# Kernel tuning notes

Measured on AMD Instinct MI355X. Metric: run time of the kernel, lower is better.

## Reference

```python
import jax, jax.numpy as jnp
import numpy as np
from jax import lax

K = 16  # knn_k


def _mlp(x, W1, b1, W2, b2):
    h = jax.nn.gelu(x @ W1 + b1, approximate=False)  # torch nn.GELU default = exact
    return h @ W2 + b2


def setup_inputs() -> dict:
    key = jax.random.key(0)
    ks = jax.random.split(key, 10)
    B, N, F, H = 8, 4096, 64, 128

    def xav(k, shape):
        fan_in = shape[0]
        return (jax.random.normal(k, shape, jnp.float32) / np.sqrt(fan_in)).astype(jnp.float32)

    return {
        "coords": jax.random.normal(ks[0], (B, N, 3), jnp.float32),
        "features": jax.random.normal(ks[1], (B, N, F), jnp.float32),
        "inv_W1": xav(ks[2], (6, H)), "inv_b1": jnp.zeros((H,), jnp.float32),
        "inv_W2": xav(ks[3], (H, H)), "inv_b2": jnp.zeros((H,), jnp.float32),
        "feat_W1": xav(ks[4], (F, H)), "feat_b1": jnp.zeros((H,), jnp.float32),
        "feat_W2": xav(ks[5], (H, H)), "feat_b2": jnp.zeros((H,), jnp.float32),
        "sh_W1": xav(ks[6], (2 * H, H)), "sh_b1": jnp.zeros((H,), jnp.float32),
        "sh_W2": xav(ks[7], (H, H)), "sh_b2": jnp.zeros((H,), jnp.float32),
        "g0_W": xav(ks[8], (H, 1)), "g0_b": jnp.zeros((1,), jnp.float32),
    }


def _local_geometry(coords):
    # coords: [B,N,3]
    B, N, _ = coords.shape
    k = min(K, N - 1)
    # squared pairwise distances (monotone in euclidean dist -> same kNN indices)
    sq = jnp.sum(coords * coords, axis=-1)                    # [B,N]
    dist2 = sq[:, :, None] + sq[:, None, :] - 2.0 * jnp.einsum("bnd,bmd->bnm", coords, coords)
    dist2 = lax.stop_gradient(dist2)
    eye = jnp.eye(N, dtype=bool)
    dist2 = jnp.where(eye[None], jnp.inf, dist2)
    _, idx = lax.top_k(-dist2, k)                             # smallest-k -> [B,N,k]
    neighbors = jax.vmap(lambda c, i: c[i])(coords, idx)      # [B,N,k,3]
    relative = neighbors - coords[:, :, None, :]              # [B,N,k,3]
    cov = jnp.einsum("bnki,bnkj->bnij", relative, relative) / float(k)  # [B,N,3,3]
    evals, evecs = jnp.linalg.eigh(cov)                       # ascending
    normals = evecs[..., 0]                                   # smallest-eigval eigenvector, [B,N,3]
    center = coords.mean(axis=1, keepdims=True)
    outward = coords - center
    orient = jnp.sign(jnp.sum(normals * outward, axis=-1, keepdims=True))
    orient = jnp.where(orient == 0, 1.0, orient)
    normals = normals * orient
    normals = normals / jnp.maximum(jnp.linalg.norm(normals, axis=-1, keepdims=True), 1e-6)
    radius = jnp.linalg.norm(relative, axis=-1).mean(axis=-1, keepdims=True)   # [B,N,1]
    centered_radius = jnp.linalg.norm(outward, axis=-1, keepdims=True)
    eig_sum = jnp.maximum(evals.sum(axis=-1, keepdims=True), 1e-6)
    dominance = evals[..., 2:3] / eig_sum
    invariants = jnp.concatenate([evals, radius, centered_radius, dominance], axis=-1)  # [B,N,6]
    return normals, invariants


def reference(coords, features, inv_W1, inv_b1, inv_W2, inv_b2,
              feat_W1, feat_b1, feat_W2, feat_b2,
              sh_W1, sh_b1, sh_W2, sh_b2, g0_W, g0_b):
    normals, invariants = _local_geometry(coords)
    inv_h = _mlp(invariants, inv_W1, inv_b1, inv_W2, inv_b2)
    feat_h = _mlp(features, feat_W1, feat_b1, feat_W2, feat_b2)
    hidden = _mlp(jnp.concatenate([inv_h, feat_h], axis=-1), sh_W1, sh_b1, sh_W2, sh_b2)
    scalar = hidden @ g0_W + g0_b                                   # grade 0, [B,N,1]
    plane = jnp.stack([normals[..., 0], normals[..., 1], -normals[..., 2],
                       -jnp.sum(coords * normals, axis=-1)], axis=-1)  # grade 1, [B,N,4]
    biv = jnp.concatenate([normals, jnp.zeros_like(normals)], axis=-1)  # grade 2, [B,N,6]
    point = jnp.concatenate([coords, jnp.ones(coords.shape[:-1] + (1,), coords.dtype)], axis=-1)  # grade 3 OPNS point
    zero4 = jnp.zeros(coords.shape[:-1] + (1,), coords.dtype)            # grade 4
    return jnp.concatenate([scalar, plane, biv, point, zero4], axis=-1)  # [B,N,16]
```

## Files before the change

kernel.cpp:

```cpp
#include <hip/hip_runtime.h>
#include <hip/hip_bf16.h>

#define BB 8
#define NN 4096
#define FF 64
#define HH 128
#define KNN 16

typedef __attribute__((ext_vector_type(8))) short bf16x8;
typedef __attribute__((ext_vector_type(4))) float f32x4;

#define OFF_iW2 0
#define OFF_fW1 16384
#define OFF_fW2 24576
#define OFF_sW1 40960
#define OFF_sW2 73728
#define HI_SZ   90112

__device__ __forceinline__ float sq3(float x, float y, float z) {
    return fmaf(z, z, fmaf(y, y, __fmul_rn(x, x)));
}
__device__ __forceinline__ float dist2f(float px, float py, float pz, float psq, float4 cc) {
    float t = fmaf(pz, cc.z, fmaf(py, cc.y, __fmul_rn(px, cc.x)));
    return __fsub_rn(__fadd_rn(psq, cc.w), __fmul_rn(2.0f, t));
}

__device__ __forceinline__ short f2bf(float x) {
    unsigned u = __float_as_uint(x);
    u += 0x7fffu + ((u >> 16) & 1u);
    return (short)(u >> 16);
}
__device__ __forceinline__ float bf2f(short s) {
    return __uint_as_float(((unsigned)(unsigned short)s) << 16);
}

extern "C" __global__ __launch_bounds__(256)
void k_prep(const float* __restrict__ coords, float4* __restrict__ coords4, float* __restrict__ center) {
    const int b = blockIdx.x, tid = threadIdx.x;
    __shared__ float rx[256], ry[256], rz[256];
    float sx = 0.f, sy = 0.f, sz = 0.f;
    for (int n = tid; n < NN; n += 256) {
        const float* c = coords + (size_t)(b * NN + n) * 3;
        float x = c[0], y = c[1], z = c[2];
        coords4[b * NN + n] = make_float4(x, y, z, sq3(x, y, z));
        sx += x; sy += y; sz += z;
    }
    rx[tid] = sx; ry[tid] = sy; rz[tid] = sz;
    __syncthreads();
    for (int s = 128; s > 0; s >>= 1) {
        if (tid < s) { rx[tid] += rx[tid + s]; ry[tid] += ry[tid + s]; rz[tid] += rz[tid + s]; }
        __syncthreads();
    }
    if (tid == 0) {
        center[b * 4 + 0] = rx[0] * (1.0f / NN);
        center[b * 4 + 1] = ry[0] * (1.0f / NN);
        center[b * 4 + 2] = rz[0] * (1.0f / NN);
    }
}

extern "C" __global__ __launch_bounds__(256)
void k_wprep(const float* __restrict__ iW2, const float* __restrict__ fW1,
             const float* __restrict__ fW2, const float* __restrict__ sW1,
             const float* __restrict__ sW2, short* __restrict__ wbf) {
    const int w = blockIdx.y;
    const float* W; int K; int off;
    if (w == 0)      { W = iW2; K = 128; off = OFF_iW2; }
    else if (w == 1) { W = fW1; K = 64;  off = OFF_fW1; }
    else if (w == 2) { W = fW2; K = 128; off = OFF_fW2; }
    else if (w == 3) { W = sW1; K = 256; off = OFF_sW1; }
    else             { W = sW2; K = 128; off = OFF_sW2; }
    short* hi = wbf + off;
    short* lo = wbf + HI_SZ + off;
    const int total = K * 128;
    for (int e = blockIdx.x * 256 + threadIdx.x; e < total; e += gridDim.x * 256) {
        int j = e & 7, lane = (e >> 3) & 63, ct = (e >> 9) & 7, kb = e >> 12;
        int k = kb * 32 + (lane >> 4) * 8 + j;
        int n = ct * 16 + (lane & 15);
        float v = W[k * 128 + n];
        short h = f2bf(v);
        float r = v - bf2f(h);
        hi[e] = h; lo[e] = f2bf(r);
    }
}

#define JROT(app, aqq, apq, arp, arq, vp0, vp1, vp2, vq0, vq1, vq2) { \
    float tau_ = (aqq - app) / (2.0f * apq); \
    float tt_ = copysignf(1.0f, tau_) / (fabsf(tau_) + sqrtf(1.0f + tau_ * tau_)); \
    if (apq == 0.0f) tt_ = 0.0f; \
    float cc_ = 1.0f / sqrtf(1.0f + tt_ * tt_); \
    float ss_ = tt_ * cc_; \
    float app_n = cc_*cc_*app - 2.0f*cc_*ss_*apq + ss_*ss_*aqq; \
    float aqq_n = ss_*ss_*app + 2.0f*cc_*ss_*apq + cc_*cc_*aqq; \
    float apq_n = cc_*ss_*(app - aqq) + (cc_*cc_ - ss_*ss_)*apq; \
    float arp_n = cc_*arp - ss_*arq; \
    float arq_n = ss_*arp + cc_*arq; \
    app = app_n; aqq = aqq_n; apq = apq_n; arp = arp_n; arq = arq_n; \
    float t0_ = cc_*vp0 - ss_*vq0, t1_ = cc_*vp1 - ss_*vq1, t2_ = cc_*vp2 - ss_*vq2; \
    vq0 = ss_*vp0 + cc_*vq0; vq1 = ss_*vp1 + cc_*vq1; vq2 = ss_*vp2 + cc_*vq2; \
    vp0 = t0_; vp1 = t1_; vp2 = t2_; }

#define SWAPF(a, b) { float sw_ = a; a = b; b = sw_; }

__device__ __forceinline__ void sort16(float (&d)[16]) {
#pragma unroll
    for (int k = 2; k <= 16; k <<= 1) {
#pragma unroll
        for (int j = k >> 1; j > 0; j >>= 1) {
#pragma unroll
            for (int i = 0; i < 16; i++) {
                int l = i ^ j;
                if (l > i) {
                    if ((i & k) == 0) {
                        float mn = fminf(d[i], d[l]);
                        d[l] = fmaxf(d[i], d[l]);
                        d[i] = mn;
                    } else {
                        float mx = fmaxf(d[i], d[l]);
                        d[l] = fminf(d[i], d[l]);
                        d[i] = mx;
                    }
                }
            }
        }
    }
}

__device__ __forceinline__ void merge16(float (&dk)[16], const float (&d)[16]) {
    float t[16];
#pragma unroll
    for (int i = 0; i < 16; i++) t[i] = fminf(dk[i], d[15 - i]);
#pragma unroll
    for (int j = 8; j > 0; j >>= 1) {
#pragma unroll
        for (int i = 0; i < 16; i++) {
            int l = i ^ j;
            if (l > i) {
                float mn = fminf(t[i], t[l]);
                t[l] = fmaxf(t[i], t[l]);
                t[i] = mn;
            }
        }
    }
#pragma unroll
    for (int i = 0; i < 16; i++) dk[i] = t[i];
}

__device__ __forceinline__ float gelu_exact(float x) {
    return 0.5f * x * (1.0f + erff(x * 0.70710678118654752440f));
}

template <int KDIM, int LDA>
__device__ __forceinline__ void gemm_small(const float* A, const float* __restrict__ W,
                                           const float* __restrict__ bias, int p0, int c0, float acc[4][4]) {
    float4 bb = *(const float4*)(bias + c0);
#pragma unroll
    for (int i = 0; i < 4; i++) { acc[i][0] = bb.x; acc[i][1] = bb.y; acc[i][2] = bb.z; acc[i][3] = bb.w; }
#pragma unroll
    for (int k = 0; k < KDIM; k++) {
        float4 w = *(const float4*)(W + k * HH + c0);
#pragma unroll
        for (int i = 0; i < 4; i++) {
            float a = A[(p0 + i) * LDA + k];
            acc[i][0] = fmaf(a, w.x, acc[i][0]);
            acc[i][1] = fmaf(a, w.y, acc[i][1]);
            acc[i][2] = fmaf(a, w.z, acc[i][2]);
            acc[i][3] = fmaf(a, w.w, acc[i][3]);
        }
    }
}

template <int KB, bool INIT>
__device__ __forceinline__ void gemm_mfma(const short* Ab, const short* __restrict__ whi,
                                          const short* __restrict__ wlo,
                                          const float* __restrict__ bias,
                                          int wid, int lane, f32x4 acc[2][2]) {
    const int m16 = lane & 15, quad = lane >> 4;
    if (INIT) {
        float b0 = bias[(wid * 2 + 0) * 16 + m16];
        float b1 = bias[(wid * 2 + 1) * 16 + m16];
        acc[0][0] = (f32x4){b0, b0, b0, b0}; acc[1][0] = acc[0][0];
        acc[0][1] = (f32x4){b1, b1, b1, b1}; acc[1][1] = acc[0][1];
    }
#pragma unroll 1
    for (int kb = 0; kb < KB; kb++) {
        bf16x8 a0 = *(const bf16x8*)(Ab + m16 * 136 + kb * 32 + quad * 8);
        bf16x8 a1 = *(const bf16x8*)(Ab + (m16 + 16) * 136 + kb * 32 + quad * 8);
#pragma unroll
        for (int c = 0; c < 2; c++) {
            const int off = ((kb * 8 + wid * 2 + c) * 64 + lane) * 8;
            bf16x8 bh = *(const bf16x8*)(whi + off);
            bf16x8 bl = *(const bf16x8*)(wlo + off);
            acc[0][c] = __builtin_amdgcn_mfma_f32_16x16x32_bf16(a0, bh, acc[0][c], 0, 0, 0);
            acc[0][c] = __builtin_amdgcn_mfma_f32_16x16x32_bf16(a0, bl, acc[0][c], 0, 0, 0);
            acc[1][c] = __builtin_amdgcn_mfma_f32_16x16x32_bf16(a1, bh, acc[1][c], 0, 0, 0);
            acc[1][c] = __builtin_amdgcn_mfma_f32_16x16x32_bf16(a1, bl, acc[1][c], 0, 0, 0);
        }
    }
}

__device__ __forceinline__ void acc_to_bf(short* dst, f32x4 acc[2][2], int wid, int lane, bool dogelu) {
    const int m16 = lane & 15, quad = lane >> 4;
#pragma unroll
    for (int mt = 0; mt < 2; mt++)
#pragma unroll
        for (int c = 0; c < 2; c++)
#pragma unroll
            for (int i = 0; i < 4; i++) {
                float v = acc[mt][c][i];
                if (dogelu) v = gelu_exact(v);
                dst[(mt * 16 + quad * 4 + i) * 136 + (wid * 2 + c) * 16 + m16] = f2bf(v);
            }
}

extern "C" __global__ __launch_bounds__(256, 7)
void k_fused(const float4* __restrict__ coords4, const float* __restrict__ center,
             const float* __restrict__ features, const short* __restrict__ wbf,
             const float* __restrict__ iW1, const float* __restrict__ ib1,
             const float* __restrict__ ib2,
             const float* __restrict__ fb1, const float* __restrict__ fb2,
             const float* __restrict__ sb1, const float* __restrict__ sb2,
             const float* __restrict__ gW, const float* __restrict__ gb,
             float* __restrict__ out) {
    const int blk = blockIdx.x;
    const int b = blk >> 7;
    const int chunk = blk & 127;
    const int tid = threadIdx.x;
    const int pid = tid & 31;
    const int h = tid >> 5;
    const int n = chunk * 32 + pid;
    const float4* __restrict__ C = coords4 + b * NN;

    __shared__ __align__(16) char smem[22144];
    float4* tile = (float4*)smem;
    short* ilist = (short*)(smem + 8192);
    int* cnts = (int*)(smem + 19968);
    float* inv8 = (float*)(smem + 20992);
    float* sc = (float*)(smem + 22016);
    float* mb = (float*)smem;
    short* Abf = (short*)smem;
    short* FHbf = (short*)(smem + 8704);

    float4 me = C[n];
    const float px = me.x, py = me.y, pz = me.z, psq = me.w;
    const float INF = __builtin_inff();

    float dk[KNN];
#pragma unroll
    for (int i = 0; i < KNN; i++) dk[i] = INF;

    for (int r = 0; r < 8; r++) {
        __syncthreads();
#pragma unroll
        for (int e = tid; e < 512; e += 256) {
            int seg = e >> 6, idx = e & 63;
            tile[e] = C[seg * 512 + r * 64 + idx];
        }
        __syncthreads();
        const float4* T = &tile[h * 64];
        const int selfj = n - (h * 512 + r * 64);
#pragma unroll
        for (int bt = 0; bt < 4; bt++) {
            float d[16];
#pragma unroll
            for (int i = 0; i < 16; i++) {
                float4 cc = T[bt * 16 + i];
                float dd = dist2f(px, py, pz, psq, cc);
                d[i] = (bt * 16 + i) == selfj ? INF : dd;
            }
            sort16(d);
            merge16(dk, d);
        }
    }

    __syncthreads();
#pragma unroll
    for (int i = 0; i < KNN; i++) mb[tid * 17 + i] = dk[i];
    __syncthreads();
#pragma unroll
    for (int p = 1; p < 8; p++) {
        const int partner = (((h + p) & 7) << 5) + pid;
        float o[16];
#pragma unroll
        for (int i = 0; i < KNN; i++) o[i] = mb[partner * 17 + i];
        merge16(dk, o);
    }
    const float d15 = dk[15];

    int cs = 0, ct = 0;
    const int lbase = (pid * 8 + h) * 23;
    for (int r = 0; r < 8; r++) {
        __syncthreads();
#pragma unroll
        for (int e = tid; e < 512; e += 256) {
            int seg = e >> 6, idx = e & 63;
            tile[e] = C[seg * 512 + r * 64 + idx];
        }
        __syncthreads();
        const float4* T = &tile[h * 64];
        const int base = h * 512 + r * 64;
#pragma unroll 4
        for (int j = 0; j < 64; j++) {
            float4 cc = T[j];
            float d = dist2f(px, py, pz, psq, cc);
            int g = base + j;
            if (g != n && d <= d15) {
                if (d < d15) {
                    if (cs < 15) ilist[lbase + cs] = (short)g;
                    cs++;
                } else if (ct < 8) {
                    ilist[lbase + 15 + ct] = (short)g;
                    ct++;
                }
            }
        }
    }
    cnts[pid * 8 + h] = (cs & 0xff) | (ct << 8);
    __syncthreads();

    if (h == 0) {
        int s[8], t8[8], sb[8], tb[8], cum[8], tcum[8];
#pragma unroll
        for (int q = 0; q < 8; q++) {
            int cp = cnts[pid * 8 + q];
            s[q] = cp & 0xff; t8[q] = cp >> 8;
            sb[q] = (pid * 8 + q) * 23; tb[q] = sb[q] + 15;
        }
        cum[0] = s[0]; tcum[0] = t8[0];
#pragma unroll
        for (int q = 1; q < 8; q++) { cum[q] = cum[q - 1] + s[q]; tcum[q] = tcum[q - 1] + t8[q]; }

        float cxx = 0.f, cxy = 0.f, cxz = 0.f, cyy = 0.f, cyz = 0.f, czz = 0.f, radsum = 0.f;
#pragma unroll
        for (int j = 0; j < KNN; j++) {
            int addr = sb[0] + j;
#pragma unroll
            for (int q = 1; q < 8; q++)
                if (j >= cum[q - 1]) addr = sb[q] + (j - cum[q - 1]);
            int jt = j - cum[7];
            if (j >= cum[7]) addr = tb[0] + jt;
#pragma unroll
            for (int q = 1; q < 8; q++)
                if (j >= cum[7] && jt >= tcum[q - 1]) addr = tb[q] + (jt - tcum[q - 1]);
            int id = ilist[addr];
            float4 cc = C[id];
            float rx = __fsub_rn(cc.x, px), ry = __fsub_rn(cc.y, py), rz = __fsub_rn(cc.z, pz);
            cxx = __fadd_rn(cxx, __fmul_rn(rx, rx));
            cxy = __fadd_rn(cxy, __fmul_rn(rx, ry));
            cxz = __fadd_rn(cxz, __fmul_rn(rx, rz));
            cyy = __fadd_rn(cyy, __fmul_rn(ry, ry));
            cyz = __fadd_rn(cyz, __fmul_rn(ry, rz));
            czz = __fadd_rn(czz, __fmul_rn(rz, rz));
            float rr = __fadd_rn(__fadd_rn(__fmul_rn(rx, rx), __fmul_rn(ry, ry)), __fmul_rn(rz, rz));
            radsum = __fadd_rn(radsum, sqrtf(rr));
        }
        const float inv_k = 1.0f / KNN;
        float a00 = cxx * inv_k, a01 = cxy * inv_k, a02 = cxz * inv_k;
        float a11 = cyy * inv_k, a12 = cyz * inv_k, a22 = czz * inv_k;

        float V00 = 1.f, V01 = 0.f, V02 = 0.f;
        float V10 = 0.f, V11 = 1.f, V12 = 0.f;
        float V20 = 0.f, V21 = 0.f, V22 = 1.f;
        for (int sweep = 0; sweep < 6; sweep++) {
            JROT(a00, a11, a01, a02, a12, V00, V10, V20, V01, V11, V21);
            JROT(a00, a22, a02, a01, a12, V00, V10, V20, V02, V12, V22);
            JROT(a11, a22, a12, a01, a02, V01, V11, V21, V02, V12, V22);
        }
        float e0 = a00, e1 = a11, e2 = a22;
        float x0 = V00, y0 = V10, z0 = V20;
        float x1 = V01, y1 = V11, z1 = V21;
        float x2 = V02, y2 = V12, z2 = V22;
        if (e0 > e1) { SWAPF(e0, e1); SWAPF(x0, x1); SWAPF(y0, y1); SWAPF(z0, z1); }
        if (e1 > e2) { SWAPF(e1, e2); SWAPF(x1, x2); SWAPF(y1, y2); SWAPF(z1, z2); }
        if (e0 > e1) { SWAPF(e0, e1); SWAPF(x0, x1); SWAPF(y0, y1); SWAPF(z0, z1); }

        float cx = center[b * 4 + 0], cy = center[b * 4 + 1], cz = center[b * 4 + 2];
        float ox = __fsub_rn(px, cx), oy = __fsub_rn(py, cy), oz = __fsub_rn(pz, cz);
        float dt = __fadd_rn(__fadd_rn(__fmul_rn(x0, ox), __fmul_rn(y0, oy)), __fmul_rn(z0, oz));
        float sgn = (dt >= 0.0f) ? 1.0f : -1.0f;
        x0 *= sgn; y0 *= sgn; z0 *= sgn;
        float nrm = sqrtf(__fadd_rn(__fadd_rn(__fmul_rn(x0, x0), __fmul_rn(y0, y0)), __fmul_rn(z0, z0)));
        float den = fmaxf(nrm, 1e-6f);
        x0 = x0 / den; y0 = y0 / den; z0 = z0 / den;

        float radius = radsum * inv_k;
        float crad = sqrtf(__fadd_rn(__fadd_rn(__fmul_rn(ox, ox), __fmul_rn(oy, oy)), __fmul_rn(oz, oz)));
        float esum = fmaxf(__fadd_rn(__fadd_rn(e0, e1), e2), 1e-6f);
        float dom = e2 / esum;

        float* ip = inv8 + pid * 8;
        ip[0] = e0; ip[1] = e1; ip[2] = e2; ip[3] = radius; ip[4] = crad; ip[5] = dom;
        ip[6] = 0.f; ip[7] = 0.f;

        float pd = __fadd_rn(__fadd_rn(__fmul_rn(px, x0), __fmul_rn(py, y0)), __fmul_rn(pz, z0));
        float4* o = (float4*)(out + (size_t)(b * NN + n) * 16);
        o[0] = make_float4(0.0f, x0, y0, -z0);
        o[1] = make_float4(-pd, x0, y0, z0);
        o[2] = make_float4(0.0f, 0.0f, 0.0f, px);
        o[3] = make_float4(py, pz, 1.0f, 0.0f);
        sc[pid] = gb[0];
    }
    __syncthreads();

    const int wid = tid >> 6, lane = tid & 63;
    const short* w_iW2h = wbf + OFF_iW2; const short* w_iW2l = wbf + HI_SZ + OFF_iW2;
    const short* w_fW1h = wbf + OFF_fW1; const short* w_fW1l = wbf + HI_SZ + OFF_fW1;
    const short* w_fW2h = wbf + OFF_fW2; const short* w_fW2l = wbf + HI_SZ + OFF_fW2;
    const short* w_sW1h = wbf + OFF_sW1; const short* w_sW1l = wbf + HI_SZ + OFF_sW1;
    const short* w_sW2h = wbf + OFF_sW2; const short* w_sW2l = wbf + HI_SZ + OFF_sW2;
    f32x4 acc[2][2];

    {
        int row = tid >> 3, c8 = (tid & 7) * 8;
        const float* s = features + (size_t)(b * NN + chunk * 32 + row) * FF + c8;
        float4 v0 = *(const float4*)s, v1 = *(const float4*)(s + 4);
        bf16x8 pk;
        pk[0] = f2bf(v0.x); pk[1] = f2bf(v0.y); pk[2] = f2bf(v0.z); pk[3] = f2bf(v0.w);
        pk[4] = f2bf(v1.x); pk[5] = f2bf(v1.y); pk[6] = f2bf(v1.z); pk[7] = f2bf(v1.w);
        *(bf16x8*)(Abf + row * 136 + c8) = pk;
    }
    __syncthreads();

    gemm_mfma<2, true>(Abf, w_fW1h, w_fW1l, fb1, wid, lane, acc);
    __syncthreads();
    acc_to_bf(Abf, acc, wid, lane, true);
    __syncthreads();

    gemm_mfma<4, true>(Abf, w_fW2h, w_fW2l, fb2, wid, lane, acc);
    __syncthreads();
    acc_to_bf(FHbf, acc, wid, lane, false);
    __syncthreads();

    {
        const int cg = tid & 31, pg = tid >> 5;
        const int c0 = cg * 4, p0 = pg * 4;
        float a4[4][4];
        gemm_small<6, 8>(inv8, iW1, ib1, p0, c0, a4);
#pragma unroll
        for (int i = 0; i < 4; i++)
#pragma unroll
            for (int j = 0; j < 4; j++)
                Abf[(p0 + i) * 136 + c0 + j] = f2bf(gelu_exact(a4[i][j]));
    }
    __syncthreads();

    gemm_mfma<4, true>(Abf, w_iW2h, w_iW2l, ib2, wid, lane, acc);
    __syncthreads();
    acc_to_bf(Abf, acc, wid, lane, false);
    __syncthreads();

    gemm_mfma<4, true>(Abf, w_sW1h, w_sW1l, sb1, wid, lane, acc);
    gemm_mfma<4, false>(FHbf, w_sW1h + 16384, w_sW1l + 16384, nullptr, wid, lane, acc);
    __syncthreads();
    acc_to_bf(Abf, acc, wid, lane, true);
    __syncthreads();

    gemm_mfma<4, true>(Abf, w_sW2h, w_sW2l, sb2, wid, lane, acc);
    {
        const int m16 = lane & 15, quad = lane >> 4;
#pragma unroll
        for (int mt = 0; mt < 2; mt++)
#pragma unroll
            for (int c = 0; c < 2; c++) {
                float g = gW[(wid * 2 + c) * 16 + m16];
#pragma unroll
                for (int i = 0; i < 4; i++)
                    atomicAdd(&sc[mt * 16 + quad * 4 + i], acc[mt][c][i] * g);
            }
    }
    __syncthreads();
    if (tid < 32) out[(size_t)(b * NN + n) * 16] = sc[tid];
}

extern "C" void kernel_launch(void* const* d_in, const int* in_sizes, int n_in,
                              void* d_out, int out_size, void* d_ws, size_t ws_size,
                              hipStream_t stream) {
    const float* coords   = (const float*)d_in[0];
    const float* features = (const float*)d_in[1];
    const float* iW1 = (const float*)d_in[2],  * ib1 = (const float*)d_in[3];
    const float* iW2 = (const float*)d_in[4],  * ib2 = (const float*)d_in[5];
    const float* fW1 = (const float*)d_in[6],  * fb1 = (const float*)d_in[7];
    const float* fW2 = (const float*)d_in[8],  * fb2 = (const float*)d_in[9];
    const float* sW1 = (const float*)d_in[10], * sb1 = (const float*)d_in[11];
    const float* sW2 = (const float*)d_in[12], * sb2 = (const float*)d_in[13];
    const float* gW  = (const float*)d_in[14], * gb  = (const float*)d_in[15];
    float* out = (float*)d_out;

    float* ws = (float*)d_ws;
    float4* coords4 = (float4*)ws;
    float* center = ws + BB * NN * 4;
    short* wbf = (short*)((char*)d_ws + 524416);

    hipLaunchKernelGGL(k_prep, dim3(BB), dim3(256), 0, stream, coords, coords4, center);
    hipLaunchKernelGGL(k_wprep, dim3(16, 5), dim3(256), 0, stream, iW2, fW1, fW2, sW1, sW2, wbf);
    hipLaunchKernelGGL(k_fused, dim3(1024), dim3(256), 0, stream, coords4, center, features, wbf,
                       iW1, ib1, ib2, fb1, fb2, sb1, sb2, gW, gb, out);
}
```

Before: 290.1 us.

## Halve points per block to 16 and split kNN scan into 16 segments

Each block now handles 16 query points instead of 32, with 16 threads per point scanning 256-candidate segments. The grid doubles to 2048 blocks, and the tile rows are padded to 33 entries. The MLP stage switches to single 16-row MFMA tiles, and the merge and gather steps are widened to 16 partial lists. The aim is more parallelism and better wave occupancy across CUs. In exchange, each block does more merge work (15 partner merges), every block reloads the weights, and half the threads sit idle during the feature load.

```diff
diff --git a/kernel.cpp b/kernel.cpp
--- a/kernel.cpp
+++ b/kernel.cpp
@@ -150,16 +150,16 @@
 }
 
 template <int KDIM, int LDA>
-__device__ __forceinline__ void gemm_small(const float* A, const float* __restrict__ W,
-                                           const float* __restrict__ bias, int p0, int c0, float acc[4][4]) {
+__device__ __forceinline__ void gemm_small2(const float* A, const float* __restrict__ W,
+                                            const float* __restrict__ bias, int p0, int c0, float acc[2][4]) {
     float4 bb = *(const float4*)(bias + c0);
 #pragma unroll
-    for (int i = 0; i < 4; i++) { acc[i][0] = bb.x; acc[i][1] = bb.y; acc[i][2] = bb.z; acc[i][3] = bb.w; }
+    for (int i = 0; i < 2; i++) { acc[i][0] = bb.x; acc[i][1] = bb.y; acc[i][2] = bb.z; acc[i][3] = bb.w; }
 #pragma unroll
     for (int k = 0; k < KDIM; k++) {
         float4 w = *(const float4*)(W + k * HH + c0);
 #pragma unroll
-        for (int i = 0; i < 4; i++) {
+        for (int i = 0; i < 2; i++) {
             float a = A[(p0 + i) * LDA + k];
             acc[i][0] = fmaf(a, w.x, acc[i][0]);
             acc[i][1] = fmaf(a, w.y, acc[i][1]);
@@ -170,46 +170,41 @@
 }
 
 template <int KB, bool INIT>
-__device__ __forceinline__ void gemm_mfma(const short* Ab, const short* __restrict__ whi,
-                                          const short* __restrict__ wlo,
-                                          const float* __restrict__ bias,
-                                          int wid, int lane, f32x4 acc[2][2]) {
+__device__ __forceinline__ void gemm_mfma16(const short* Ab, const short* __restrict__ whi,
+                                            const short* __restrict__ wlo,
+                                            const float* __restrict__ bias,
+                                            int wid, int lane, f32x4 acc[2]) {
     const int m16 = lane & 15, quad = lane >> 4;
     if (INIT) {
         float b0 = bias[(wid * 2 + 0) * 16 + m16];
         float b1 = bias[(wid * 2 + 1) * 16 + m16];
-        acc[0][0] = (f32x4){b0, b0, b0, b0}; acc[1][0] = acc[0][0];
-        acc[0][1] = (f32x4){b1, b1, b1, b1}; acc[1][1] = acc[0][1];
+        acc[0] = (f32x4){b0, b0, b0, b0};
+        acc[1] = (f32x4){b1, b1, b1, b1};
     }
 #pragma unroll 1
     for (int kb = 0; kb < KB; kb++) {
         bf16x8 a0 = *(const bf16x8*)(Ab + m16 * 136 + kb * 32 + quad * 8);
-        bf16x8 a1 = *(const bf16x8*)(Ab + (m16 + 16) * 136 + kb * 32 + quad * 8);
 #pragma unroll
         for (int c = 0; c < 2; c++) {
             const int off = ((kb * 8 + wid * 2 + c) * 64 + lane) * 8;
             bf16x8 bh = *(const bf16x8*)(whi + off);
             bf16x8 bl = *(const bf16x8*)(wlo + off);
-            acc[0][c] = __builtin_amdgcn_mfma_f32_16x16x32_bf16(a0, bh, acc[0][c], 0, 0, 0);
-            acc[0][c] = __builtin_amdgcn_mfma_f32_16x16x32_bf16(a0, bl, acc[0][c], 0, 0, 0);
-            acc[1][c] = __builtin_amdgcn_mfma_f32_16x16x32_bf16(a1, bh, acc[1][c], 0, 0, 0);
-            acc[1][c] = __builtin_amdgcn_mfma_f32_16x16x32_bf16(a1, bl, acc[1][c], 0, 0, 0);
-        }
-    }
-}
-
-__device__ __forceinline__ void acc_to_bf(short* dst, f32x4 acc[2][2], int wid, int lane, bool dogelu) {
+            acc[c] = __builtin_amdgcn_mfma_f32_16x16x32_bf16(a0, bh, acc[c], 0, 0, 0);
+            acc[c] = __builtin_amdgcn_mfma_f32_16x16x32_bf16(a0, bl, acc[c], 0, 0, 0);
+        }
+    }
+}
+
+__device__ __forceinline__ void acc_to_bf(short* dst, f32x4 acc[2], int wid, int lane, bool dogelu) {
     const int m16 = lane & 15, quad = lane >> 4;
 #pragma unroll
-    for (int mt = 0; mt < 2; mt++)
-#pragma unroll
-        for (int c = 0; c < 2; c++)
-#pragma unroll
-            for (int i = 0; i < 4; i++) {
-                float v = acc[mt][c][i];
-                if (dogelu) v = gelu_exact(v);
-                dst[(mt * 16 + quad * 4 + i) * 136 + (wid * 2 + c) * 16 + m16] = f2bf(v);
-            }
+    for (int c = 0; c < 2; c++)
+#pragma unroll
+        for (int i = 0; i < 4; i++) {
+            float v = acc[c][i];
+            if (dogelu) v = gelu_exact(v);
+            dst[(quad * 4 + i) * 136 + (wid * 2 + c) * 16 + m16] = f2bf(v);
+        }
 }
 
 extern "C" __global__ __launch_bounds__(256, 7)
@@ -222,23 +217,23 @@
              const float* __restrict__ gW, const float* __restrict__ gb,
              float* __restrict__ out) {
     const int blk = blockIdx.x;
-    const int b = blk >> 7;
-    const int chunk = blk & 127;
+    const int b = blk >> 8;
+    const int chunk = blk & 255;
     const int tid = threadIdx.x;
-    const int pid = tid & 31;
-    const int h = tid >> 5;
-    const int n = chunk * 32 + pid;
+    const int pid = tid & 15;
+    const int h = tid >> 4;
+    const int n = chunk * 16 + pid;
     const float4* __restrict__ C = coords4 + b * NN;
 
-    __shared__ __align__(16) char smem[22144];
+    __shared__ __align__(16) char smem[21824];
     float4* tile = (float4*)smem;
-    short* ilist = (short*)(smem + 8192);
-    int* cnts = (int*)(smem + 19968);
-    float* inv8 = (float*)(smem + 20992);
-    float* sc = (float*)(smem + 22016);
+    short* ilist = (short*)(smem + 8448);
+    int* cnts = (int*)(smem + 20224);
+    float* inv8 = (float*)(smem + 21248);
+    float* sc = (float*)(smem + 21760);
     float* mb = (float*)smem;
     short* Abf = (short*)smem;
-    short* FHbf = (short*)(smem + 8704);
+    short* FHbf = (short*)(smem + 4352);
 
     float4 me = C[n];
     const float px = me.x, py = me.y, pz = me.z, psq = me.w;
@@ -252,14 +247,14 @@
         __syncthreads();
 #pragma unroll
         for (int e = tid; e < 512; e += 256) {
-            int seg = e >> 6, idx = e & 63;
-            tile[e] = C[seg * 512 + r * 64 + idx];
+            int seg = e >> 5, idx = e & 31;
+            tile[seg * 33 + idx] = C[seg * 256 + r * 32 + idx];
         }
         __syncthreads();
-        const float4* T = &tile[h * 64];
-        const int selfj = n - (h * 512 + r * 64);
-#pragma unroll
-        for (int bt = 0; bt < 4; bt++) {
+        const float4* T = &tile[h * 33];
+        const int selfj = n - (h * 256 + r * 32);
+#pragma unroll
+        for (int bt = 0; bt < 2; bt++) {
             float d[16];
 #pragma unroll
             for (int i = 0; i < 16; i++) {
@@ -277,8 +272,8 @@
     for (int i = 0; i < KNN; i++) mb[tid * 17 + i] = dk[i];
     __syncthreads();
 #pragma unroll
-    for (int p = 1; p < 8; p++) {
-        const int partner = (((h + p) & 7) << 5) + pid;
+    for (int p = 1; p < 16; p++) {
+        const int partner = (((h + p) & 15) << 4) + pid;
         float o[16];
 #pragma unroll
         for (int i = 0; i < KNN; i++) o[i] = mb[partner * 17 + i];
@@ -287,19 +282,19 @@
     const float d15 = dk[15];
 
     int cs = 0, ct = 0;
-    const int lbase = (pid * 8 + h) * 23;
+    const int lbase = (pid * 16 + h) * 23;
     for (int r = 0; r < 8; r++) {
         __syncthreads();
 #pragma unroll
         for (int e = tid; e < 512; e += 256) {
-            int seg = e >> 6, idx = e & 63;
-            tile[e] = C[seg * 512 + r * 64 + idx];
+            int seg = e >> 5, idx = e & 31;
+            tile[seg * 33 + idx] = C[seg * 256 + r * 32 + idx];
         }
         __syncthreads();
-        const float4* T = &tile[h * 64];
-        const int base = h * 512 + r * 64;
+        const float4* T = &tile[h * 33];
+        const int base = h * 256 + r * 32;
 #pragma unroll 4
-        for (int j = 0; j < 64; j++) {
+        for (int j = 0; j < 32; j++) {
             float4 cc = T[j];
             float d = dist2f(px, py, pz, psq, cc);
             int g = base + j;
@@ -314,33 +309,33 @@
             }
         }
     }
-    cnts[pid * 8 + h] = (cs & 0xff) | (ct << 8);
+    cnts[pid * 16 + h] = (cs & 0xff) | (ct << 8);
     __syncthreads();
 
     if (h == 0) {
-        int s[8], t8[8], sb[8], tb[8], cum[8], tcum[8];
-#pragma unroll
-        for (int q = 0; q < 8; q++) {
-            int cp = cnts[pid * 8 + q];
+        int s[16], t8[16], sb[16], tb[16], cum[16], tcum[16];
+#pragma unroll
+        for (int q = 0; q < 16; q++) {
+            int cp = cnts[pid * 16 + q];
             s[q] = cp & 0xff; t8[q] = cp >> 8;
-            sb[q] = (pid * 8 + q) * 23; tb[q] = sb[q] + 15;
+            sb[q] = (pid * 16 + q) * 23; tb[q] = sb[q] + 15;
         }
         cum[0] = s[0]; tcum[0] = t8[0];
 #pragma unroll
-        for (int q = 1; q < 8; q++) { cum[q] = cum[q - 1] + s[q]; tcum[q] = tcum[q - 1] + t8[q]; }
+        for (int q = 1; q < 16; q++) { cum[q] = cum[q - 1] + s[q]; tcum[q] = tcum[q - 1] + t8[q]; }
 
         float cxx = 0.f, cxy = 0.f, cxz = 0.f, cyy = 0.f, cyz = 0.f, czz = 0.f, radsum = 0.f;
 #pragma unroll
         for (int j = 0; j < KNN; j++) {
             int addr = sb[0] + j;
 #pragma unroll
-            for (int q = 1; q < 8; q++)
+            for (int q = 1; q < 16; q++)
                 if (j >= cum[q - 1]) addr = sb[q] + (j - cum[q - 1]);
-            int jt = j - cum[7];
-            if (j >= cum[7]) addr = tb[0] + jt;
-#pragma unroll
-            for (int q = 1; q < 8; q++)
-                if (j >= cum[7] && jt >= tcum[q - 1]) addr = tb[q] + (jt - tcum[q - 1]);
+            int jt = j - cum[15];
+            if (j >= cum[15]) addr = tb[0] + jt;
+#pragma unroll
+            for (int q = 1; q < 16; q++)
+                if (j >= cum[15] && jt >= tcum[q - 1]) addr = tb[q] + (jt - tcum[q - 1]);
             int id = ilist[addr];
             float4 cc = C[id];
             float rx = __fsub_rn(cc.x, px), ry = __fsub_rn(cc.y, py), rz = __fsub_rn(cc.z, pz);
@@ -407,11 +402,11 @@
     const short* w_fW2h = wbf + OFF_fW2; const short* w_fW2l = wbf + HI_SZ + OFF_fW2;
     const short* w_sW1h = wbf + OFF_sW1; const short* w_sW1l = wbf + HI_SZ + OFF_sW1;
     const short* w_sW2h = wbf + OFF_sW2; const short* w_sW2l = wbf + HI_SZ + OFF_sW2;
-    f32x4 acc[2][2];
-
-    {
+    f32x4 acc[2];
+
+    if (tid < 128) {
         int row = tid >> 3, c8 = (tid & 7) * 8;
-        const float* s = features + (size_t)(b * NN + chunk * 32 + row) * FF + c8;
+        const float* s = features + (size_t)(b * NN + chunk * 16 + row) * FF + c8;
         float4 v0 = *(const float4*)s, v1 = *(const float4*)(s + 4);
         bf16x8 pk;
         pk[0] = f2bf(v0.x); pk[1] = f2bf(v0.y); pk[2] = f2bf(v0.z); pk[3] = f2bf(v0.w);
@@ -420,55 +415,53 @@
     }
     __syncthreads();
 
-    gemm_mfma<2, true>(Abf, w_fW1h, w_fW1l, fb1, wid, lane, acc);
+    gemm_mfma16<2, true>(Abf, w_fW1h, w_fW1l, fb1, wid, lane, acc);
     __syncthreads();
     acc_to_bf(Abf, acc, wid, lane, true);
     __syncthreads();
 
-    gemm_mfma<4, true>(Abf, w_fW2h, w_fW2l, fb2, wid, lane, acc);
+    gemm_mfma16<4, true>(Abf, w_fW2h, w_fW2l, fb2, wid, lane, acc);
     __syncthreads();
     acc_to_bf(FHbf, acc, wid, lane, false);
     __syncthreads();
 
     {
         const int cg = tid & 31, pg = tid >> 5;
-        const int c0 = cg * 4, p0 = pg * 4;
-        float a4[4][4];
-        gemm_small<6, 8>(inv8, iW1, ib1, p0, c0, a4);
-#pragma unroll
-        for (int i = 0; i < 4; i++)
+        const int c0 = cg * 4, p0 = pg * 2;
+        float a4[2][4];
+        gemm_small2<6, 8>(inv8, iW1, ib1, p0, c0, a4);
+#pragma unroll
+        for (int i = 0; i < 2; i++)
 #pragma unroll
             for (int j = 0; j < 4; j++)
                 Abf[(p0 + i) * 136 + c0 + j] = f2bf(gelu_exact(a4[i][j]));
     }
     __syncthreads();
 
-    gemm_mfma<4, true>(Abf, w_iW2h, w_iW2l, ib2, wid, lane, acc);
+    gemm_mfma16<4, true>(Abf, w_iW2h, w_iW2l, ib2, wid, lane, acc);
     __syncthreads();
     acc_to_bf(Abf, acc, wid, lane, false);
     __syncthreads();
 
-    gemm_mfma<4, true>(Abf, w_sW1h, w_sW1l, sb1, wid, lane, acc);
-    gemm_mfma<4, false>(FHbf, w_sW1h + 16384, w_sW1l + 16384, nullptr, wid, lane, acc);
+    gemm_mfma16<4, true>(Abf, w_sW1h, w_sW1l, sb1, wid, lane, acc);
+    gemm_mfma16<4, false>(FHbf, w_sW1h + 16384, w_sW1l + 16384, nullptr, wid, lane, acc);
     __syncthreads();
     acc_to_bf(Abf, acc, wid, lane, true);
     __syncthreads();
 
-    gemm_mfma<4, true>(Abf, w_sW2h, w_sW2l, sb2, wid, lane, acc);
+    gemm_mfma16<4, true>(Abf, w_sW2h, w_sW2l, sb2, wid, lane, acc);
     {
         const int m16 = lane & 15, quad = lane >> 4;
 #pragma unroll
-        for (int mt = 0; mt < 2; mt++)
-#pragma unroll
-            for (int c = 0; c < 2; c++) {
-                float g = gW[(wid * 2 + c) * 16 + m16];
-#pragma unroll
-                for (int i = 0; i < 4; i++)
-                    atomicAdd(&sc[mt * 16 + quad * 4 + i], acc[mt][c][i] * g);
-            }
-    }
-    __syncthreads();
-    if (tid < 32) out[(size_t)(b * NN + n) * 16] = sc[tid];
+        for (int c = 0; c < 2; c++) {
+            float g = gW[(wid * 2 + c) * 16 + m16];
+#pragma unroll
+            for (int i = 0; i < 4; i++)
+                atomicAdd(&sc[quad * 4 + i], acc[c][i] * g);
+        }
+    }
+    __syncthreads();
+    if (tid < 16) out[(size_t)(b * NN + chunk * 16 + tid) * 16] = sc[tid];
 }
 
 extern "C" void kernel_launch(void* const* d_in, const int* in_sizes, int n_in,
@@ -492,6 +485,6 @@
 
     hipLaunchKernelGGL(k_prep, dim3(BB), dim3(256), 0, stream, coords, coords4, center);
     hipLaunchKernelGGL(k_wprep, dim3(16, 5), dim3(256), 0, stream, iW2, fW1, fW2, sW1, sW2, wbf);
-    hipLaunchKernelGGL(k_fused, dim3(1024), dim3(256), 0, stream, coords4, center, features, wbf,
+    hipLaunchKernelGGL(k_fused, dim3(2048), dim3(256), 0, stream, coords4, center, features, wbf,
                        iW1, ib1, ib2, fb1, fb2, sb1, sb2, gW, gb, out);
 }
```

New measurement: 316.9 us. 9.2% more time.
